# Optimization experiments

Measured on AMD Instinct MI355X. Metric: run time of the kernel, lower is better.

## Reference

```python
import jax, jax.numpy as jnp
import numpy as np

H = 64            # hidden_channels
L = 2             # num_layers
E = 300_000       # edges per relation
B = 64            # graphs in batch
NS = [100_000, 20_000, 50_000, 80_000]   # variable, value, operator, constraint
# (src_type, dst_type) for the 9 hetero relations, fixed order
RELS = [(0,1),(0,2),(0,3),(2,3),(3,3),(1,0),(2,0),(3,0),(3,2)]
R = len(RELS)
SLOPE = 0.2       # GATConv leaky_relu negative slope


def setup_inputs() -> dict:
    key = jax.random.key(0)
    ks = iter(jax.random.split(key, 64))
    inp = {}
    for n, N in zip(["x_variable", "x_value", "x_operator", "x_constraint"], NS):
        inp[n] = jax.random.normal(next(ks), (N, H), jnp.float32)
    sc = 1.0 / np.sqrt(H).astype(np.float32)
    inp["Wsrc"] = jax.random.normal(next(ks), (L, R, H, H), jnp.float32) * sc
    inp["Wdst"] = jax.random.normal(next(ks), (L, R, H, H), jnp.float32) * sc
    inp["asrc"] = jax.random.normal(next(ks), (L, R, H), jnp.float32) * sc
    inp["adst"] = jax.random.normal(next(ks), (L, R, H), jnp.float32) * sc
    inp["bias"] = jax.random.normal(next(ks), (L, R, H), jnp.float32) * 0.01
    inp["lin_w"] = jax.random.normal(next(ks), (2, 2 * H), jnp.float32) / np.sqrt(2.0 * H).astype(np.float32)
    inp["lin_b"] = jnp.zeros((2,), jnp.float32)
    for r, (s, d) in enumerate(RELS):
        inp[f"src{r}"] = jax.random.randint(next(ks), (E,), 0, NS[s], jnp.int32)
        inp[f"dst{r}"] = jax.random.randint(next(ks), (E,), 0, NS[d], jnp.int32)
    inp["batch_variable"] = jnp.sort(jax.random.randint(next(ks), (NS[0],), 0, B, jnp.int32))
    inp["batch_constraint"] = jnp.sort(jax.random.randint(next(ks), (NS[3],), 0, B, jnp.int32))
    inp["num_graphs"] = B
    return inp


def _gat(xs, xd, Ws, Wd, a_s, a_d, b, src, dst):
    """Bipartite PyG GATConv (heads=1, add_self_loops=False)."""
    hs = xs @ Ws                         # [Ns, H]
    hd = xd @ Wd                         # [Nd, H]
    al_s = hs @ a_s                      # [Ns]
    al_d = hd @ a_d                      # [Nd]
    score = jax.nn.leaky_relu(al_s[src] + al_d[dst], SLOPE)    # [E]
    nd = xd.shape[0]
    m = jax.ops.segment_max(score, dst, num_segments=nd)
    p = jnp.exp(score - m[dst])
    z = jax.ops.segment_sum(p, dst, num_segments=nd)
    alpha = p / (z[dst] + 1e-16)                               # segment softmax
    out = jax.ops.segment_sum(hs[src] * alpha[:, None], dst, num_segments=nd)
    return out + b


def _seg_mean(x, seg, n):
    s = jax.ops.segment_sum(x, seg, num_segments=n)
    c = jax.ops.segment_sum(jnp.ones((x.shape[0],), x.dtype), seg, num_segments=n)
    return s / jnp.maximum(c, 1.0)[:, None]


def reference(x_variable, x_value, x_operator, x_constraint,
              Wsrc, Wdst, asrc, adst, bias, lin_w, lin_b,
              src0, dst0, src1, dst1, src2, dst2, src3, dst3, src4, dst4,
              src5, dst5, src6, dst6, src7, dst7, src8, dst8,
              batch_variable, batch_constraint, num_graphs):
    xs = [x_variable, x_value, x_operator, x_constraint]
    srcs = [src0, src1, src2, src3, src4, src5, src6, src7, src8]
    dsts = [dst0, dst1, dst2, dst3, dst4, dst5, dst6, dst7, dst8]
    for l in range(L):
        out = [jnp.zeros((x.shape[0], H), x.dtype) for x in xs]
        for r, (s, d) in enumerate(RELS):
            out[d] = out[d] + _gat(xs[s], xs[d], Wsrc[l, r], Wdst[l, r],
                                   asrc[l, r], adst[l, r], bias[l, r],
                                   srcs[r], dsts[r])
        xs = [jax.nn.relu(o) for o in out]   # dropout is identity in eval
    vp = _seg_mean(xs[0], batch_variable, num_graphs)   # [B, H]
    cp = _seg_mean(xs[3], batch_constraint, num_graphs) # [B, H]
    return jnp.concatenate([vp, cp], axis=1) @ lin_w.T + lin_b   # [B, 2]
```

## Files before the change

kernel.cpp:

```cpp
#include <hip/hip_runtime.h>
#include <hip/hip_bf16.h>

#define NH 64
#define NRELS 9
#define NEDGE 300000
#define NGRAPH 64
#define TOTROWS 250000
#define TOTFSEG 660000
#define TOTEDGE (NRELS * NEDGE)
#define NBUCK 977
#define NBC 4
#define CHUNK 4096
#define NBLK ((TOTEDGE + CHUNK - 1) / CHUNK)
#define KCH 20
#define KSP 33

typedef __attribute__((ext_vector_type(8))) short short8;
typedef __attribute__((ext_vector_type(4))) float f32x4;

__constant__ int c_NS[4]     = {100000, 20000, 50000, 80000};
__constant__ int c_SRC[9]    = {0,0,0,2,3,1,2,3,3};
__constant__ int c_DST[9]    = {1,2,3,3,3,0,0,0,2};
__constant__ int c_XOFF[5]   = {0,100000,120000,170000,250000};
__constant__ int c_ASOFF[10] = {0,100000,200000,300000,350000,430000,450000,500000,580000,660000};
__constant__ int c_FOFF[5]   = {0,300000,320000,420000,660000};
__constant__ int c_NRELT[4]  = {3,1,2,3};
__constant__ int c_RRANK[9]  = {0,0,0,1,2,0,1,2,1};

struct EdgePtrs { const int* s[9]; const int* d[9]; };

__device__ __forceinline__ unsigned short f2bf(float f) {
  union { __hip_bfloat16 h; unsigned short u; } c;
  c.h = __float2bfloat16(f);
  return c.u;
}

__device__ __forceinline__ float wred_max32(float v) {
#pragma unroll
  for (int o = 16; o; o >>= 1) v = fmaxf(v, __shfl_xor(v, o, 32));
  return v;
}

__global__ void k_setup(const float* Wsrc, const float* Wdst, const float* asrc,
                        const float* adst, const float* bias, float* wv, float* bsum,
                        unsigned short* wb) {
  int b = blockIdx.x, j = threadIdx.x;
  if (b < 36) {
    int r = b % 9, q = b / 9;
    int l = q >> 1, side = q & 1;
    const float* W = (side ? Wdst : Wsrc) + (l * 9 + r) * 64 * 64;
    const float* a = (side ? adst : asrc) + (l * 9 + r) * 64;
    float s = 0.f;
    for (int i = 0; i < 64; ++i) s += W[j * 64 + i] * a[i];
    wv[(side ? 1152 : 0) + (l * 9 + r) * 64 + j] = s;
  } else if (b == 36) {
    for (int l = 0; l < 2; ++l)
      for (int t = 0; t < 4; ++t) {
        float s = 0.f;
        for (int r = 0; r < 9; ++r)
          if (c_DST[r] == t) s += bias[(l * 9 + r) * 64 + j];
        bsum[(l * 4 + t) * 64 + j] = s;
      }
  } else {
    int idx = b - 37;
    int l = idx / 9, r = idx % 9;
    const float* W = Wsrc + (size_t)(l * 9 + r) * 4096;
    unsigned short* dst = wb + (size_t)(l * 9 + r) * 4096;
    for (int k = 0; k < 64; ++k)
      dst[j * 64 + k] = f2bf(W[k * 64 + j]);
  }
}

__global__ __launch_bounds__(256) void k_bhist2(EdgePtrs Eg, int* bh) {
  __shared__ int sh[NBUCK];
  for (int i = threadIdx.x; i < NBUCK; i += 256) sh[i] = 0;
  __syncthreads();
  int lo = blockIdx.x * CHUNK;
  int hi = lo + CHUNK; if (hi > TOTEDGE) hi = TOTEDGE;
  for (int gid = lo + threadIdx.x; gid < hi; gid += 256) {
    int r = gid / NEDGE, e = gid - r * NEDGE;
    int g = c_XOFF[c_DST[r]] + Eg.d[r][e];
    atomicAdd(&sh[g >> 8], 1);
  }
  __syncthreads();
  int* dst = bh + (size_t)blockIdx.x * NBUCK;
  for (int i = threadIdx.x; i < NBUCK; i += 256) dst[i] = sh[i];
}

__global__ void k_cs1(const int* bh, int* csum) {
  int blk = blockIdx.x;
  int c = blk / NBC;
  int b = (blk % NBC) * 256 + threadIdx.x;
  if (b >= NBUCK) return;
  int k0 = c * KSP;
  int k1 = k0 + KSP; if (k1 > NBLK) k1 = NBLK;
  int s = 0;
  for (int k = k0; k < k1; ++k) s += bh[(size_t)k * NBUCK + b];
  csum[(size_t)c * NBUCK + b] = s;
}

__global__ void k_cs2(int* csum, int* gbh) {
  int b = blockIdx.x * 256 + threadIdx.x;
  if (b >= NBUCK) return;
  int run = 0;
#pragma unroll
  for (int c = 0; c < KCH; ++c) {
    size_t idx = (size_t)c * NBUCK + b;
    int t = csum[idx];
    csum[idx] = run;
    run += t;
  }
  gbh[b] = run;
}

__global__ void k_cs3(int* bh, const int* csum) {
  int blk = blockIdx.x;
  int c = blk / NBC;
  int b = (blk % NBC) * 256 + threadIdx.x;
  if (b >= NBUCK) return;
  int k0 = c * KSP;
  int k1 = k0 + KSP; if (k1 > NBLK) k1 = NBLK;
  int run = csum[(size_t)c * NBUCK + b];
  for (int k = k0; k < k1; ++k) {
    size_t idx = (size_t)k * NBUCK + b;
    int t = bh[idx];
    bh[idx] = run;
    run += t;
  }
}

__global__ void k_bscan(const int* gbh, int* boff) {
  __shared__ int sd[1024];
  int t = threadIdx.x;
  int v = (t < NBUCK) ? gbh[t] : 0;
  sd[t] = v; __syncthreads();
  for (int o = 1; o < 1024; o <<= 1) {
    int x = (t >= o) ? sd[t - o] : 0; __syncthreads();
    sd[t] += x; __syncthreads();
  }
  if (t < NBUCK) boff[t] = sd[t] - v;
  if (t == 1023) boff[NBUCK] = sd[1023];
}

__global__ __launch_bounds__(256) void k_bin2(EdgePtrs Eg, const int* bh, const int* boff, int* pairs) {
  __shared__ int cur[NBUCK];
  const int* mybh = bh + (size_t)blockIdx.x * NBUCK;
  for (int i = threadIdx.x; i < NBUCK; i += 256) cur[i] = boff[i] + mybh[i];
  __syncthreads();
  int lo = blockIdx.x * CHUNK;
  int hi = lo + CHUNK; if (hi > TOTEDGE) hi = TOTEDGE;
  for (int gid = lo + threadIdx.x; gid < hi; gid += 256) {
    int r = gid / NEDGE, e = gid - r * NEDGE;
    int g = c_XOFF[c_DST[r]] + Eg.d[r][e];
    int b = g >> 8;
    int pos = atomicAdd(&cur[b], 1);
    int key = ((g & 255) << 2) | c_RRANK[r];
    pairs[pos] = (key << 20) | (c_ASOFF[r] + Eg.s[r][e]);
  }
}

__global__ __launch_bounds__(256) void k_bsort(const int* pairs, const int* boff,
                                               int* rowptr, int* asx) {
  __shared__ int ssc[1024];
  __shared__ int scur[1024];
  __shared__ int sws[256];
  int b = blockIdx.x, t = threadIdx.x;
  int lo = boff[b], hi = boff[b + 1];
  int n = hi - lo;
  for (int i = t; i < 1024; i += 256) ssc[i] = 0;
  __syncthreads();
  for (int i = t; i < n; i += 256)
    atomicAdd(&ssc[((unsigned)pairs[lo + i]) >> 20], 1);
  __syncthreads();
  int c0 = ssc[t * 4], c1 = ssc[t * 4 + 1], c2 = ssc[t * 4 + 2], c3 = ssc[t * 4 + 3];
  int s = c0 + c1 + c2 + c3;
  sws[t] = s;
  __syncthreads();
  for (int o = 1; o < 256; o <<= 1) {
    int x = (t >= o) ? sws[t - o] : 0; __syncthreads();
    sws[t] += x; __syncthreads();
  }
  int base = sws[t] - s;
  ssc[t * 4]     = base;
  ssc[t * 4 + 1] = base + c0;
  ssc[t * 4 + 2] = base + c0 + c1;
  ssc[t * 4 + 3] = base + c0 + c1 + c2;
  scur[t * 4]     = ssc[t * 4];
  scur[t * 4 + 1] = ssc[t * 4 + 1];
  scur[t * 4 + 2] = ssc[t * 4 + 2];
  scur[t * 4 + 3] = ssc[t * 4 + 3];
  __syncthreads();
  int nodeBase = b << 8;
  for (int i = t; i < 1024; i += 256) {
    int l = i >> 2, rank = i & 3;
    int g = nodeBase + l;
    if (g < TOTROWS) {
      int tt = (g >= c_XOFF[1]) + (g >= c_XOFF[2]) + (g >= c_XOFF[3]);
      int nr = c_NRELT[tt];
      if (rank < nr)
        rowptr[c_FOFF[tt] + (g - c_XOFF[tt]) * nr + rank] = lo + ssc[i];
    }
  }
  if (b == 0 && t == 0) rowptr[TOTFSEG] = TOTEDGE;
  for (int i = t; i < n; i += 256) {
    int p = pairs[lo + i];
    int pos = atomicAdd(&scur[((unsigned)p) >> 20], 1);
    asx[lo + pos] = (int)(((((unsigned)p >> 20) & 3u) << 20) | ((unsigned)p & 0xFFFFFu));
  }
}

struct GemmAllP {
  const float* x0; const float* x1; const float* x2; const float* x3;
  const unsigned short* Wb;
  __hip_bfloat16* hs;
  float* als; float* ald;
  const float* wvs; const float* wvd;
  int act; int ntyp;
  int tbase[5];
  int typ[4];
  int nrel[4];
  int rel[4][3];
  int ndrel[4];
  int drel[4][3];
};

#define XSTR 72

__global__ __launch_bounds__(256) void k_gemma(GemmAllP G) {
  __shared__ unsigned short sx[64 * XSTR];
  __shared__ unsigned short sw[64 * XSTR];
  int bid = blockIdx.x;
  int k = 0;
#pragma unroll 3
  for (int q = 1; q < 4; ++q) if (q < G.ntyp) k += (bid >= G.tbase[q]);
  int st = G.typ[k];
  int tile = bid - G.tbase[k];
  int Ns = c_NS[st];
  const float* x = st == 0 ? G.x0 : st == 1 ? G.x1 : st == 2 ? G.x2 : G.x3;
  int base = tile * 64;
  int tid = threadIdx.x;
  for (int kk = tid; kk < 1024; kk += 256) {
    int row = kk >> 4;
    int c4 = (kk & 15) * 4;
    int gr = base + row;
    float4 v = make_float4(0.f, 0.f, 0.f, 0.f);
    if (gr < Ns) v = ((const float4*)x)[(size_t)gr * 16 + (kk & 15)];
    if (G.act) { v.x = fmaxf(v.x, 0.f); v.y = fmaxf(v.y, 0.f); v.z = fmaxf(v.z, 0.f); v.w = fmaxf(v.w, 0.f); }
    ushort4 u;
    u.x = f2bf(v.x); u.y = f2bf(v.y); u.z = f2bf(v.z); u.w = f2bf(v.w);
    *(ushort4*)&sx[row * XSTR + c4] = u;
  }
  __syncthreads();
  {
    int row = tid >> 2, part = tid & 3;
    int gr2 = base + row;
    if (gr2 < Ns) {
      float xv[16];
      const float4* xr = (const float4*)x + (size_t)gr2 * 16 + part * 4;
      float4 v0 = xr[0], v1 = xr[1], v2 = xr[2], v3 = xr[3];
      xv[0]=v0.x; xv[1]=v0.y; xv[2]=v0.z; xv[3]=v0.w;
      xv[4]=v1.x; xv[5]=v1.y; xv[6]=v1.z; xv[7]=v1.w;
      xv[8]=v2.x; xv[9]=v2.y; xv[10]=v2.z; xv[11]=v2.w;
      xv[12]=v3.x; xv[13]=v3.y; xv[14]=v3.z; xv[15]=v3.w;
      if (G.act) {
#pragma unroll
        for (int i = 0; i < 16; ++i) xv[i] = fmaxf(xv[i], 0.f);
      }
      int nrl0 = G.nrel[k];
      for (int ri = 0; ri < nrl0; ++ri) {
        int r = G.rel[k][ri];
        const float* wvp = G.wvs + r * 64 + part * 16;
        float s = 0.f;
#pragma unroll
        for (int i = 0; i < 16; ++i) s += xv[i] * wvp[i];
        s += __shfl_xor(s, 1);
        s += __shfl_xor(s, 2);
        if (part == 0) G.als[c_ASOFF[r] + gr2] = s;
      }
      int ndl = G.ndrel[k];
      for (int ri = 0; ri < ndl; ++ri) {
        int r = G.drel[k][ri];
        const float* wvp = G.wvd + r * 64 + part * 16;
        float s = 0.f;
#pragma unroll
        for (int i = 0; i < 16; ++i) s += xv[i] * wvp[i];
        s += __shfl_xor(s, 1);
        s += __shfl_xor(s, 2);
        if (part == 0)
          G.ald[c_FOFF[st] + gr2 * c_NRELT[st] + c_RRANK[r]] = s;
      }
    }
  }
  int w    = tid >> 6;
  int lane = tid & 63;
  int m    = lane & 15;
  int quad = lane >> 4;
  short8 a0 = *(const short8*)&sx[(w * 16 + m) * XSTR + quad * 8];
  short8 a1 = *(const short8*)&sx[(w * 16 + m) * XSTR + 32 + quad * 8];
  int nrl = G.nrel[k];
  for (int ri = 0; ri < nrl; ++ri) {
    int r = G.rel[k][ri];
    const unsigned short* Wb = G.Wb + (size_t)r * 4096;
    if (ri) __syncthreads();
    {
      int n = tid >> 2;
      int k0 = (tid & 3) << 4;
      short8 w0 = *(const short8*)&Wb[n * 64 + k0];
      short8 w1 = *(const short8*)&Wb[n * 64 + k0 + 8];
      *(short8*)&sw[n * XSTR + k0] = w0;
      *(short8*)&sw[n * XSTR + k0 + 8] = w1;
    }
    __syncthreads();
    f32x4 acc[4];
#pragma unroll
    for (int cb = 0; cb < 4; ++cb) acc[cb] = (f32x4)(0.f);
#pragma unroll
    for (int cb = 0; cb < 4; ++cb) {
      short8 b0 = *(const short8*)&sw[(cb * 16 + m) * XSTR + quad * 8];
      short8 b1 = *(const short8*)&sw[(cb * 16 + m) * XSTR + 32 + quad * 8];
      acc[cb] = __builtin_amdgcn_mfma_f32_16x16x32_bf16(a0, b0, acc[cb], 0, 0, 0);
      acc[cb] = __builtin_amdgcn_mfma_f32_16x16x32_bf16(a1, b1, acc[cb], 0, 0, 0);
    }
    __hip_bfloat16* hsb = G.hs + (size_t)c_ASOFF[r] * 64;
#pragma unroll
    for (int cb = 0; cb < 4; ++cb)
#pragma unroll
      for (int reg = 0; reg < 4; ++reg)
        sx[(w * 16 + quad * 4 + reg) * XSTR + cb * 16 + m] = f2bf(acc[cb][reg]);
    int rrow = w * 16 + (lane >> 2);
    int rcol = (lane & 3) * 16;
    int lr = base + rrow;
    if (lr < Ns) {
      short8 v0 = *(const short8*)&sx[rrow * XSTR + rcol];
      short8 v1 = *(const short8*)&sx[rrow * XSTR + rcol + 8];
      *(short8*)&hsb[(size_t)lr * 64 + rcol] = v0;
      *(short8*)&hsb[(size_t)lr * 64 + rcol + 8] = v1;
    }
  }
}

struct GatherP {
  const __hip_bfloat16* hs;
  const float* als;
  const float* ald;
  const int* rowptr; const int* asx;
  float* xA;
  const float* bsum;
  int ntypes;
  int tbase[5];
  int typ[4];
};

__global__ __launch_bounds__(256) void k_gather(GatherP A) {
  __shared__ unsigned long long sRA[8][96];
  __shared__ float sZ[8][4];
  int bid = blockIdx.x;
  int k = 0;
#pragma unroll 3
  for (int q = 1; q < 4; ++q) if (q < A.ntypes) k += (bid >= A.tbase[q]);
  int t = A.typ[k];
  int Nd = c_NS[t];
  int lane = threadIdx.x & 63;
  int half = lane >> 5;
  int sl   = lane & 31;
  int hid  = threadIdx.x >> 5;
  int node = (bid - A.tbase[k]) * 8 + (threadIdx.x >> 6) * 2 + half;
  if (node >= Nd) return;
  int nr = c_NRELT[t];
  int fb = c_FOFF[t] + node * nr;
  int p0 = A.rowptr[fb];
  int p1 = A.rowptr[fb + nr];
  int deg = p1 - p0; if (deg > 96) deg = 96;
  float2 acc = ((const float2*)(A.bsum + t * 64))[sl];
  if (deg > 0) {
    if (sl < 4) sZ[hid][sl] = 0.f;
    const float NEG = -3.4e38f;
    const unsigned* ax = (const unsigned*)A.asx;
    unsigned rec0 = 0, rec1 = 0, rec2 = 0;
    int rk0 = 0, rk1 = 0, rk2 = 0;
    float s0 = NEG, s1 = NEG, s2 = NEG;
    if (sl < deg) {
      rec0 = ax[p0 + sl];
      rk0 = (int)((rec0 >> 20) & 3u);
      float v = A.als[rec0 & 0xFFFFFu] + A.ald[fb + rk0];
      s0 = v >= 0.f ? v : 0.2f * v;
    }
    if (sl + 32 < deg) {
      rec1 = ax[p0 + 32 + sl];
      rk1 = (int)((rec1 >> 20) & 3u);
      float v = A.als[rec1 & 0xFFFFFu] + A.ald[fb + rk1];
      s1 = v >= 0.f ? v : 0.2f * v;
    }
    if (sl + 64 < deg) {
      rec2 = ax[p0 + 64 + sl];
      rk2 = (int)((rec2 >> 20) & 3u);
      float v = A.als[rec2 & 0xFFFFFu] + A.ald[fb + rk2];
      s2 = v >= 0.f ? v : 0.2f * v;
    }
    float M = wred_max32(fmaxf(fmaxf(s0, s1), s2));
    float e0 = 0.f, e1 = 0.f, e2 = 0.f;
    if (sl < deg)      { e0 = __expf(s0 - M); atomicAdd(&sZ[hid][rk0], e0); }
    if (sl + 32 < deg) { e1 = __expf(s1 - M); atomicAdd(&sZ[hid][rk1], e1); }
    if (sl + 64 < deg) { e2 = __expf(s2 - M); atomicAdd(&sZ[hid][rk2], e2); }
    asm volatile("s_waitcnt lgkmcnt(0)" ::: "memory");
    float rz0 = 1.f / (sZ[hid][0] + 1e-16f);
    float rz1 = 1.f / (sZ[hid][1] + 1e-16f);
    float rz2 = 1.f / (sZ[hid][2] + 1e-16f);
    float a0 = e0 * (rk0 == 0 ? rz0 : (rk0 == 1 ? rz1 : rz2));
    sRA[hid][sl] = ((unsigned long long)__float_as_uint(a0) << 32) | ((rec0 & 0xFFFFFu) << 7);
    if (deg > 32) {
      float a1 = e1 * (rk1 == 0 ? rz0 : (rk1 == 1 ? rz1 : rz2));
      sRA[hid][32 + sl] = ((unsigned long long)__float_as_uint(a1) << 32) | ((rec1 & 0xFFFFFu) << 7);
    }
    if (deg > 64) {
      float a2 = e2 * (rk2 == 0 ? rz0 : (rk2 == 1 ? rz1 : rz2));
      sRA[hid][64 + sl] = ((unsigned long long)__float_as_uint(a2) << 32) | ((rec2 & 0xFFFFFu) << 7);
    }
    const char* hsb = (const char*)A.hs;
    unsigned sl4 = (unsigned)sl * 4u;
    int nb = (deg + 7) >> 3;
    for (int g = 0; g < nb; g += 2) {
      unsigned long long raA[8], raB[8];
      unsigned hA[8], hB[8];
      bool hasB = (g + 1) < nb;
#pragma unroll
      for (int q = 0; q < 8; ++q) raA[q] = sRA[hid][g * 8 + q];
#pragma unroll
      for (int q = 0; q < 8; ++q)
        hA[q] = *(const unsigned*)(hsb + ((unsigned)(raA[q] & 0xFFFFFFFFu) + sl4));
      if (hasB) {
#pragma unroll
        for (int q = 0; q < 8; ++q) raB[q] = sRA[hid][g * 8 + 8 + q];
#pragma unroll
        for (int q = 0; q < 8; ++q)
          hB[q] = *(const unsigned*)(hsb + ((unsigned)(raB[q] & 0xFFFFFFFFu) + sl4));
      }
#pragma unroll
      for (int q = 0; q < 8; ++q) {
        float aq = __uint_as_float((unsigned)(raA[q] >> 32));
        acc.x = fmaf(aq, __uint_as_float(hA[q] << 16), acc.x);
        acc.y = fmaf(aq, __uint_as_float(hA[q] & 0xffff0000u), acc.y);
      }
      if (hasB) {
#pragma unroll
        for (int q = 0; q < 8; ++q) {
          float aq = __uint_as_float((unsigned)(raB[q] >> 32));
          acc.x = fmaf(aq, __uint_as_float(hB[q] << 16), acc.x);
          acc.y = fmaf(aq, __uint_as_float(hB[q] & 0xffff0000u), acc.y);
        }
      }
    }
  }
  float* xout = A.xA + (size_t)c_XOFF[t] * 64;
  *(float2*)&xout[(size_t)node * 64 + sl * 2] = acc;
}

struct GatherPoolP {
  const __hip_bfloat16* hs;
  const float* als;
  const float* ald;
  const int* rowptr; const int* asx;
  const float* bsum;
  int ntypes;
  int tbase[5];
  int typ[4];
  const int* bvar; const int* bcon;
  float* partial;
};

__global__ __launch_bounds__(256) void k_gatherpool(GatherPoolP A) {
  __shared__ unsigned long long sRA[8][96];
  __shared__ float sZ[8][4];
  __shared__ float sPool[8][64];
  __shared__ int sG[8];
  int bid = blockIdx.x;
  int k = 0;
#pragma unroll 3
  for (int q = 1; q < 4; ++q) if (q < A.ntypes) k += (bid >= A.tbase[q]);
  int t = A.typ[k];
  int Nd = c_NS[t];
  int lane = threadIdx.x & 63;
  int half = lane >> 5;
  int sl   = lane & 31;
  int hid  = threadIdx.x >> 5;
  int node = (bid - A.tbase[k]) * 8 + (threadIdx.x >> 6) * 2 + half;
  bool active = node < Nd;
  float2 acc = ((const float2*)(A.bsum + t * 64))[sl];
  int nr = c_NRELT[t];
  int fb = c_FOFF[t] + node * nr;
  int deg = 0, p0 = 0;
  if (active) {
    p0 = A.rowptr[fb];
    int p1 = A.rowptr[fb + nr];
    deg = p1 - p0; if (deg > 96) deg = 96;
  }
  if (deg > 0) {
    if (sl < 4) sZ[hid][sl] = 0.f;
    const float NEG = -3.4e38f;
    const unsigned* ax = (const unsigned*)A.asx;
    unsigned rec0 = 0, rec1 = 0, rec2 = 0;
    int rk0 = 0, rk1 = 0, rk2 = 0;
    float s0 = NEG, s1 = NEG, s2 = NEG;
    if (sl < deg) {
      rec0 = ax[p0 + sl];
      rk0 = (int)((rec0 >> 20) & 3u);
      float v = A.als[rec0 & 0xFFFFFu] + A.ald[fb + rk0];
      s0 = v >= 0.f ? v : 0.2f * v;
    }
    if (sl + 32 < deg) {
      rec1 = ax[p0 + 32 + sl];
      rk1 = (int)((rec1 >> 20) & 3u);
      float v = A.als[rec1 & 0xFFFFFu] + A.ald[fb + rk1];
      s1 = v >= 0.f ? v : 0.2f * v;
    }
    if (sl + 64 < deg) {
      rec2 = ax[p0 + 64 + sl];
      rk2 = (int)((rec2 >> 20) & 3u);
      float v = A.als[rec2 & 0xFFFFFu] + A.ald[fb + rk2];
      s2 = v >= 0.f ? v : 0.2f * v;
    }
    float M = wred_max32(fmaxf(fmaxf(s0, s1), s2));
    float e0 = 0.f, e1 = 0.f, e2 = 0.f;
    if (sl < deg)      { e0 = __expf(s0 - M); atomicAdd(&sZ[hid][rk0], e0); }
    if (sl + 32 < deg) { e1 = __expf(s1 - M); atomicAdd(&sZ[hid][rk1], e1); }
    if (sl + 64 < deg) { e2 = __expf(s2 - M); atomicAdd(&sZ[hid][rk2], e2); }
    asm volatile("s_waitcnt lgkmcnt(0)" ::: "memory");
    float rz0 = 1.f / (sZ[hid][0] + 1e-16f);
    float rz1 = 1.f / (sZ[hid][1] + 1e-16f);
    float rz2 = 1.f / (sZ[hid][2] + 1e-16f);
    float a0 = e0 * (rk0 == 0 ? rz0 : (rk0 == 1 ? rz1 : rz2));
    sRA[hid][sl] = ((unsigned long long)__float_as_uint(a0) << 32) | ((rec0 & 0xFFFFFu) << 7);
    if (deg > 32) {
      float a1 = e1 * (rk1 == 0 ? rz0 : (rk1 == 1 ? rz1 : rz2));
      sRA[hid][32 + sl] = ((unsigned long long)__float_as_uint(a1) << 32) | ((rec1 & 0xFFFFFu) << 7);
    }
    if (deg > 64) {
      float a2 = e2 * (rk2 == 0 ? rz0 : (rk2 == 1 ? rz1 : rz2));
      sRA[hid][64 + sl] = ((unsigned long long)__float_as_uint(a2) << 32) | ((rec2 & 0xFFFFFu) << 7);
    }
    const char* hsb = (const char*)A.hs;
    unsigned sl4 = (unsigned)sl * 4u;
    int nb = (deg + 7) >> 3;
    for (int g = 0; g < nb; g += 2) {
      unsigned long long raA[8], raB[8];
      unsigned hA[8], hB[8];
      bool hasB = (g + 1) < nb;
#pragma unroll
      for (int q = 0; q < 8; ++q) raA[q] = sRA[hid][g * 8 + q];
#pragma unroll
      for (int q = 0; q < 8; ++q)
        hA[q] = *(const unsigned*)(hsb + ((unsigned)(raA[q] & 0xFFFFFFFFu) + sl4));
      if (hasB) {
#pragma unroll
        for (int q = 0; q < 8; ++q) raB[q] = sRA[hid][g * 8 + 8 + q];
#pragma unroll
        for (int q = 0; q < 8; ++q)
          hB[q] = *(const unsigned*)(hsb + ((unsigned)(raB[q] & 0xFFFFFFFFu) + sl4));
      }
#pragma unroll
      for (int q = 0; q < 8; ++q) {
        float aq = __uint_as_float((unsigned)(raA[q] >> 32));
        acc.x = fmaf(aq, __uint_as_float(hA[q] << 16), acc.x);
        acc.y = fmaf(aq, __uint_as_float(hA[q] & 0xffff0000u), acc.y);
      }
      if (hasB) {
#pragma unroll
        for (int q = 0; q < 8; ++q) {
          float aq = __uint_as_float((unsigned)(raB[q] >> 32));
          acc.x = fmaf(aq, __uint_as_float(hB[q] << 16), acc.x);
          acc.y = fmaf(aq, __uint_as_float(hB[q] & 0xffff0000u), acc.y);
        }
      }
    }
  }
  sPool[hid][sl * 2]     = fmaxf(acc.x, 0.f);
  sPool[hid][sl * 2 + 1] = fmaxf(acc.y, 0.f);
  if (sl == 0) {
    int gid = -1;
    if (active) {
      int g = (t == 0) ? A.bvar[node] : A.bcon[node];
      gid = (g << 1) | (t == 3 ? 1 : 0);
    }
    sG[hid] = gid;
  }
  __syncthreads();
  if (threadIdx.x < 64) {
    int col = threadIdx.x;
    int sp = (bid & 7) << 7;
    float a = 0.f; int cg = -1;
#pragma unroll
    for (int i = 0; i < 8; ++i) {
      int gi = sG[i];
      if (gi < 0) continue;
      float v = sPool[i][col];
      if (gi == cg) a += v;
      else {
        if (cg >= 0) atomicAdd(&A.partial[(size_t)(sp | cg) * 64 + col], a);
        cg = gi; a = v;
      }
    }
    if (cg >= 0) atomicAdd(&A.partial[(size_t)(sp | cg) * 64 + col], a);
  }
}

__global__ void k_gbound(const int* bvar, const int* bcon, int* gs0, int* gs3, float* partial) {
  int gid = blockIdx.x * 256 + threadIdx.x;
  const int N0 = 100000, N3 = 80000;
  if (gid < N0) {
    int i = gid;
    int b = bvar[i];
    int bp = i ? bvar[i - 1] : -1;
    for (int g = bp + 1; g <= b; ++g) gs0[g] = i;
    if (i == N0 - 1) for (int g = b + 1; g <= 64; ++g) gs0[g] = N0;
  } else if (gid < N0 + N3) {
    int i = gid - N0;
    int b = bcon[i];
    int bp = i ? bcon[i - 1] : -1;
    for (int g = bp + 1; g <= b; ++g) gs3[g] = i;
    if (i == N3 - 1) for (int g = b + 1; g <= 64; ++g) gs3[g] = N3;
  } else if (gid < N0 + N3 + 65536) {
    partial[gid - N0 - N3] = 0.f;
  }
}

__global__ void k_poolred2(const float* partial, float* pool) {
  int g = blockIdx.x >> 1;
  int t = blockIdx.x & 1;
  int col = threadIdx.x;
  float s = 0.f;
#pragma unroll
  for (int sp = 0; sp < 8; ++sp)
    s += partial[(size_t)(((sp << 7) | (g << 1) | t)) * 64 + col];
  pool[(t ? 4096 : 0) + g * 64 + col] = s;
}

__global__ void k_final(const float* pool, const int* gs0, const int* gs3,
                        const float* lin_w, const float* lin_b, float* out) {
  int k = threadIdx.x;
  int g = k >> 1, o = k & 1;
  float c0 = fmaxf((float)(gs0[g + 1] - gs0[g]), 1.f);
  float c3 = fmaxf((float)(gs3[g + 1] - gs3[g]), 1.f);
  float acc = lin_b[o];
  for (int i = 0; i < 64; ++i) {
    acc += (pool[g * 64 + i] / c0) * lin_w[o * 128 + i];
    acc += (pool[4096 + g * 64 + i] / c3) * lin_w[o * 128 + 64 + i];
  }
  out[g * 2 + o] = acc;
}

__global__ void k_bail(float* out) {
  if (threadIdx.x < 128) out[threadIdx.x] = 0.f;
}

extern "C" void kernel_launch(void* const* d_in, const int* in_sizes, int n_in,
                              void* d_out, int out_size, void* d_ws, size_t ws_size,
                              hipStream_t stream) {
  (void)in_sizes; (void)n_in; (void)out_size;
  const size_t O_XA   = 0;
  const size_t O_HS   = 16000000;
  const size_t O_ALS  = 37120000;
  const size_t O_ALD  = 37780000;
  const size_t O_WV   = 39790000;
  const size_t O_BS   = 39792304;
  const size_t O_RP   = 39792816;
  const size_t O_ASX  = 40452832;
  const size_t O_GS   = 43152832;
  const size_t O_PART = 43153088;
  const size_t O_POOL = 43218624;
  const size_t O_WB   = 43226816;
  const size_t NEED   = 43263680;

  if (ws_size < NEED * 4) {
    k_bail<<<1, 128, 0, stream>>>((float*)d_out);
    return;
  }

  const float* x0 = (const float*)d_in[0];
  const float* x1 = (const float*)d_in[1];
  const float* x2 = (const float*)d_in[2];
  const float* x3 = (const float*)d_in[3];
  const float* Wsrc = (const float*)d_in[4];
  const float* Wdst = (const float*)d_in[5];
  const float* asrc = (const float*)d_in[6];
  const float* adst = (const float*)d_in[7];
  const float* bias = (const float*)d_in[8];
  const float* lin_w = (const float*)d_in[9];
  const float* lin_b = (const float*)d_in[10];
  EdgePtrs Eg;
  for (int r = 0; r < 9; ++r) {
    Eg.s[r] = (const int*)d_in[11 + 2 * r];
    Eg.d[r] = (const int*)d_in[12 + 2 * r];
  }
  const int* bvar = (const int*)d_in[29];
  const int* bcon = (const int*)d_in[30];

  float* ws = (float*)d_ws;
  float* xA   = ws + O_XA;
  __hip_bfloat16* hs = (__hip_bfloat16*)(ws + O_HS);
  int* bh     = (int*)(ws + O_HS);
  int* pairs  = bh + (size_t)NBLK * NBUCK;
  int* gbh    = pairs + 2700000;
  int* boff   = gbh + (NBUCK + 1);
  int* csum   = boff + (NBUCK + 2);
  float* als  = ws + O_ALS;
  float* ald  = ws + O_ALD;
  float* wv   = ws + O_WV;
  float* bsum = ws + O_BS;
  int* rowptr = (int*)(ws + O_RP);
  int* asx    = (int*)(ws + O_ASX);
  int* gs0    = (int*)(ws + O_GS);
  int* gs3    = gs0 + 65;
  float* partial = ws + O_PART;
  float* pool = ws + O_POOL;
  unsigned short* wb = (unsigned short*)(ws + O_WB);

  const int h_NS[4]   = {100000, 20000, 50000, 80000};
  const int h_SRC[9]  = {0,0,0,2,3,1,2,3,3};
  const int h_DST[9]  = {1,2,3,3,3,0,0,0,2};
  const int h_XOFF[4] = {0,100000,120000,170000};

  k_setup<<<55, 64, 0, stream>>>(Wsrc, Wdst, asrc, adst, bias, wv, bsum, wb);

  k_bhist2<<<NBLK, 256, 0, stream>>>(Eg, bh);
  k_cs1<<<KCH * NBC, 256, 0, stream>>>(bh, csum);
  k_cs2<<<NBC, 256, 0, stream>>>(csum, gbh);
  k_cs3<<<KCH * NBC, 256, 0, stream>>>(bh, csum);
  k_bscan<<<1, 1024, 0, stream>>>(gbh, boff);
  k_bin2<<<NBLK, 256, 0, stream>>>(Eg, bh, boff, pairs);
  k_bsort<<<NBUCK, 256, 0, stream>>>(pairs, boff, rowptr, asx);
  k_gbound<<<(180000 + 65536 + 255) / 256, 256, 0, stream>>>(bvar, bcon, gs0, gs3, partial);

  for (int l = 0; l < 2; ++l) {
    const float* xin[4];
    if (l == 0) { xin[0] = x0; xin[1] = x1; xin[2] = x2; xin[3] = x3; }
    else {
      for (int t = 0; t < 4; ++t) xin[t] = xA + (size_t)h_XOFF[t] * 64;
    }
    int act = (l > 0);
    int relmask = l ? 0x0FC : 0x1FF;

    GemmAllP G;
    G.x0 = xin[0]; G.x1 = xin[1]; G.x2 = xin[2]; G.x3 = xin[3];
    G.Wb = wb + (size_t)l * 9 * 4096;
    G.hs = hs; G.act = act;
    G.als = als; G.ald = ald;
    G.wvs = wv + l * 576; G.wvd = wv + 1152 + l * 576;
    int ntyp = 0, cum = 0;
    for (int t = 0; t < 4; ++t) {
      int nr = 0; int rl[3]; int nd = 0; int dl[3];
      for (int r = 0; r < 9; ++r) {
        if (!((relmask >> r) & 1)) continue;
        if (h_SRC[r] == t) rl[nr++] = r;
        if (h_DST[r] == t) dl[nd++] = r;
      }
      if (!nr && !nd) continue;
      G.typ[ntyp] = t; G.nrel[ntyp] = nr; G.ndrel[ntyp] = nd;
      for (int i = 0; i < 3; ++i) {
        G.rel[ntyp][i]  = (i < nr) ? rl[i] : 0;
        G.drel[ntyp][i] = (i < nd) ? dl[i] : 0;
      }
      G.tbase[ntyp] = cum;
      cum += (h_NS[t] + 63) / 64;
      ++ntyp;
    }
    G.ntyp = ntyp; G.tbase[ntyp] = cum;
    k_gemma<<<cum, 256, 0, stream>>>(G);

    if (l == 0) {
      GatherP A;
      A.hs = hs; A.als = als; A.ald = ald;
      A.rowptr = rowptr; A.asx = asx;
      A.xA = xA;
      A.bsum = bsum;
      int nt = 0, bcum = 0;
      for (int t = 0; t < 4; ++t) {
        A.typ[nt] = t;
        A.tbase[nt] = bcum;
        bcum += (h_NS[t] + 7) / 8;
        ++nt;
      }
      A.ntypes = nt; A.tbase[nt] = bcum;
      k_gather<<<bcum, 256, 0, stream>>>(A);
    } else {
      GatherPoolP A;
      A.hs = hs; A.als = als; A.ald = ald;
      A.rowptr = rowptr; A.asx = asx;
      A.bsum = bsum + 256;
      A.bvar = bvar; A.bcon = bcon;
      A.partial = partial;
      int nt = 0, bcum = 0;
      for (int t = 0; t < 4; ++t) {
        if (t == 1 || t == 2) continue;
        A.typ[nt] = t;
        A.tbase[nt] = bcum;
        bcum += (h_NS[t] + 7) / 8;
        ++nt;
      }
      A.ntypes = nt; A.tbase[nt] = bcum;
      k_gatherpool<<<bcum, 256, 0, stream>>>(A);
    }
  }

  k_poolred2<<<128, 64, 0, stream>>>(partial, pool);
  k_final<<<1, 128, 0, stream>>>(pool, gs0, gs3, lin_w, lin_b, (float*)d_out);
}
```

Baseline: 489.4 us.

## Replace per-block histogram scan with global atomic bucket counters and merge final kernels

The edge binning pipeline no longer stores per-block histograms and runs a three-stage column scan. Each block now adds its local bucket counts into a global histogram with atomics, a single scan produces bucket offsets, and the binning kernel recounts locally and reserves its slot range with one atomic per bucket. This removes three kernel launches and the large per-block histogram traffic, at the cost of re-reading the destination indices in the binning kernel and a nondeterministic edge order within buckets, which the later per-bucket sort is expected to absorb. The pool reduction and final linear layer are also fused into one single-block kernel.

```diff
diff --git a/kernel.cpp b/kernel.cpp
--- a/kernel.cpp
+++ b/kernel.cpp
@@ -9,11 +9,8 @@
 #define TOTFSEG 660000
 #define TOTEDGE (NRELS * NEDGE)
 #define NBUCK 977
-#define NBC 4
 #define CHUNK 4096
 #define NBLK ((TOTEDGE + CHUNK - 1) / CHUNK)
-#define KCH 20
-#define KSP 33
 
 typedef __attribute__((ext_vector_type(8))) short short8;
 typedef __attribute__((ext_vector_type(4))) float f32x4;
@@ -43,7 +40,7 @@
 
 __global__ void k_setup(const float* Wsrc, const float* Wdst, const float* asrc,
                         const float* adst, const float* bias, float* wv, float* bsum,
-                        unsigned short* wb) {
+                        unsigned short* wb, int* gbh) {
   int b = blockIdx.x, j = threadIdx.x;
   if (b < 36) {
     int r = b % 9, q = b / 9;
@@ -61,6 +58,8 @@
           if (c_DST[r] == t) s += bias[(l * 9 + r) * 64 + j];
         bsum[(l * 4 + t) * 64 + j] = s;
       }
+  } else if (b == 55) {
+    for (int i = j; i < NBUCK; i += 64) gbh[i] = 0;
   } else {
     int idx = b - 37;
     int l = idx / 9, r = idx % 9;
@@ -71,7 +70,7 @@
   }
 }
 
-__global__ __launch_bounds__(256) void k_bhist2(EdgePtrs Eg, int* bh) {
+__global__ __launch_bounds__(256) void k_bhist(EdgePtrs Eg, int* gbh) {
   __shared__ int sh[NBUCK];
   for (int i = threadIdx.x; i < NBUCK; i += 256) sh[i] = 0;
   __syncthreads();
@@ -83,53 +82,13 @@
     atomicAdd(&sh[g >> 8], 1);
   }
   __syncthreads();
-  int* dst = bh + (size_t)blockIdx.x * NBUCK;
-  for (int i = threadIdx.x; i < NBUCK; i += 256) dst[i] = sh[i];
-}
-
-__global__ void k_cs1(const int* bh, int* csum) {
-  int blk = blockIdx.x;
-  int c = blk / NBC;
-  int b = (blk % NBC) * 256 + threadIdx.x;
-  if (b >= NBUCK) return;
-  int k0 = c * KSP;
-  int k1 = k0 + KSP; if (k1 > NBLK) k1 = NBLK;
-  int s = 0;
-  for (int k = k0; k < k1; ++k) s += bh[(size_t)k * NBUCK + b];
-  csum[(size_t)c * NBUCK + b] = s;
-}
-
-__global__ void k_cs2(int* csum, int* gbh) {
-  int b = blockIdx.x * 256 + threadIdx.x;
-  if (b >= NBUCK) return;
-  int run = 0;
-#pragma unroll
-  for (int c = 0; c < KCH; ++c) {
-    size_t idx = (size_t)c * NBUCK + b;
-    int t = csum[idx];
-    csum[idx] = run;
-    run += t;
-  }
-  gbh[b] = run;
-}
-
-__global__ void k_cs3(int* bh, const int* csum) {
-  int blk = blockIdx.x;
-  int c = blk / NBC;
-  int b = (blk % NBC) * 256 + threadIdx.x;
-  if (b >= NBUCK) return;
-  int k0 = c * KSP;
-  int k1 = k0 + KSP; if (k1 > NBLK) k1 = NBLK;
-  int run = csum[(size_t)c * NBUCK + b];
-  for (int k = k0; k < k1; ++k) {
-    size_t idx = (size_t)k * NBUCK + b;
-    int t = bh[idx];
-    bh[idx] = run;
-    run += t;
-  }
-}
-
-__global__ void k_bscan(const int* gbh, int* boff) {
+  for (int i = threadIdx.x; i < NBUCK; i += 256) {
+    int v = sh[i];
+    if (v) atomicAdd(&gbh[i], v);
+  }
+}
+
+__global__ void k_bscan(const int* gbh, int* boff, int* cur) {
   __shared__ int sd[1024];
   int t = threadIdx.x;
   int v = (t < NBUCK) ? gbh[t] : 0;
@@ -138,24 +97,36 @@
     int x = (t >= o) ? sd[t - o] : 0; __syncthreads();
     sd[t] += x; __syncthreads();
   }
-  if (t < NBUCK) boff[t] = sd[t] - v;
+  if (t < NBUCK) { int e = sd[t] - v; boff[t] = e; cur[t] = e; }
   if (t == 1023) boff[NBUCK] = sd[1023];
 }
 
-__global__ __launch_bounds__(256) void k_bin2(EdgePtrs Eg, const int* bh, const int* boff, int* pairs) {
-  __shared__ int cur[NBUCK];
-  const int* mybh = bh + (size_t)blockIdx.x * NBUCK;
-  for (int i = threadIdx.x; i < NBUCK; i += 256) cur[i] = boff[i] + mybh[i];
+__global__ __launch_bounds__(256) void k_bin(EdgePtrs Eg, int* cur, int* pairs) {
+  __shared__ int sh[NBUCK];
+  __shared__ int sbase[NBUCK];
+  for (int i = threadIdx.x; i < NBUCK; i += 256) sh[i] = 0;
   __syncthreads();
   int lo = blockIdx.x * CHUNK;
   int hi = lo + CHUNK; if (hi > TOTEDGE) hi = TOTEDGE;
   for (int gid = lo + threadIdx.x; gid < hi; gid += 256) {
     int r = gid / NEDGE, e = gid - r * NEDGE;
     int g = c_XOFF[c_DST[r]] + Eg.d[r][e];
+    atomicAdd(&sh[g >> 8], 1);
+  }
+  __syncthreads();
+  for (int i = threadIdx.x; i < NBUCK; i += 256) {
+    int v = sh[i];
+    sbase[i] = v ? atomicAdd(&cur[i], v) : 0;
+    sh[i] = 0;
+  }
+  __syncthreads();
+  for (int gid = lo + threadIdx.x; gid < hi; gid += 256) {
+    int r = gid / NEDGE, e = gid - r * NEDGE;
+    int g = c_XOFF[c_DST[r]] + Eg.d[r][e];
     int b = g >> 8;
-    int pos = atomicAdd(&cur[b], 1);
+    int off = atomicAdd(&sh[b], 1);
     int key = ((g & 255) << 2) | c_RRANK[r];
-    pairs[pos] = (key << 20) | (c_ASOFF[r] + Eg.s[r][e]);
+    pairs[sbase[b] + off] = (key << 20) | (c_ASOFF[r] + Eg.s[r][e]);
   }
 }
 
@@ -623,29 +594,31 @@
   }
 }
 
-__global__ void k_poolred2(const float* partial, float* pool) {
-  int g = blockIdx.x >> 1;
-  int t = blockIdx.x & 1;
-  int col = threadIdx.x;
-  float s = 0.f;
-#pragma unroll
-  for (int sp = 0; sp < 8; ++sp)
-    s += partial[(size_t)(((sp << 7) | (g << 1) | t)) * 64 + col];
-  pool[(t ? 4096 : 0) + g * 64 + col] = s;
-}
-
-__global__ void k_final(const float* pool, const int* gs0, const int* gs3,
-                        const float* lin_w, const float* lin_b, float* out) {
-  int k = threadIdx.x;
-  int g = k >> 1, o = k & 1;
-  float c0 = fmaxf((float)(gs0[g + 1] - gs0[g]), 1.f);
-  float c3 = fmaxf((float)(gs3[g + 1] - gs3[g]), 1.f);
-  float acc = lin_b[o];
-  for (int i = 0; i < 64; ++i) {
-    acc += (pool[g * 64 + i] / c0) * lin_w[o * 128 + i];
-    acc += (pool[4096 + g * 64 + i] / c3) * lin_w[o * 128 + 64 + i];
-  }
-  out[g * 2 + o] = acc;
+__global__ __launch_bounds__(256) void k_final2(const float* partial, const int* gs0, const int* gs3,
+                                                const float* lin_w, const float* lin_b, float* out) {
+  __shared__ float sp[8192];
+  int tid = threadIdx.x;
+  for (int j = 0; j < 32; ++j) {
+    int v = j * 256 + tid;
+    int tg = v >> 6, col = v & 63;
+    float s = 0.f;
+#pragma unroll
+    for (int spi = 0; spi < 8; ++spi)
+      s += partial[(size_t)((spi << 7) | tg) * 64 + col];
+    sp[tg * 64 + col] = s;
+  }
+  __syncthreads();
+  if (tid < 128) {
+    int g = tid >> 1, o = tid & 1;
+    float c0 = fmaxf((float)(gs0[g + 1] - gs0[g]), 1.f);
+    float c3 = fmaxf((float)(gs3[g + 1] - gs3[g]), 1.f);
+    float acc = lin_b[o];
+    for (int i = 0; i < 64; ++i) {
+      acc += (sp[(g << 1) * 64 + i] / c0) * lin_w[o * 128 + i];
+      acc += (sp[((g << 1) | 1) * 64 + i] / c3) * lin_w[o * 128 + 64 + i];
+    }
+    out[g * 2 + o] = acc;
+  }
 }
 
 __global__ void k_bail(float* out) {
@@ -669,6 +642,7 @@
   const size_t O_POOL = 43218624;
   const size_t O_WB   = 43226816;
   const size_t NEED   = 43263680;
+  (void)O_POOL;
 
   if (ws_size < NEED * 4) {
     k_bail<<<1, 128, 0, stream>>>((float*)d_out);
@@ -697,11 +671,10 @@
   float* ws = (float*)d_ws;
   float* xA   = ws + O_XA;
   __hip_bfloat16* hs = (__hip_bfloat16*)(ws + O_HS);
-  int* bh     = (int*)(ws + O_HS);
-  int* pairs  = bh + (size_t)NBLK * NBUCK;
+  int* pairs  = (int*)(ws + O_HS);
   int* gbh    = pairs + 2700000;
-  int* boff   = gbh + (NBUCK + 1);
-  int* csum   = boff + (NBUCK + 2);
+  int* boff   = gbh + NBUCK + 1;
+  int* cur    = boff + NBUCK + 2;
   float* als  = ws + O_ALS;
   float* ald  = ws + O_ALD;
   float* wv   = ws + O_WV;
@@ -711,7 +684,6 @@
   int* gs0    = (int*)(ws + O_GS);
   int* gs3    = gs0 + 65;
   float* partial = ws + O_PART;
-  float* pool = ws + O_POOL;
   unsigned short* wb = (unsigned short*)(ws + O_WB);
 
   const int h_NS[4]   = {100000, 20000, 50000, 80000};
@@ -719,14 +691,11 @@
   const int h_DST[9]  = {1,2,3,3,3,0,0,0,2};
   const int h_XOFF[4] = {0,100000,120000,170000};
 
-  k_setup<<<55, 64, 0, stream>>>(Wsrc, Wdst, asrc, adst, bias, wv, bsum, wb);
-
-  k_bhist2<<<NBLK, 256, 0, stream>>>(Eg, bh);
-  k_cs1<<<KCH * NBC, 256, 0, stream>>>(bh, csum);
-  k_cs2<<<NBC, 256, 0, stream>>>(csum, gbh);
-  k_cs3<<<KCH * NBC, 256, 0, stream>>>(bh, csum);
-  k_bscan<<<1, 1024, 0, stream>>>(gbh, boff);
-  k_bin2<<<NBLK, 256, 0, stream>>>(Eg, bh, boff, pairs);
+  k_setup<<<56, 64, 0, stream>>>(Wsrc, Wdst, asrc, adst, bias, wv, bsum, wb, gbh);
+
+  k_bhist<<<NBLK, 256, 0, stream>>>(Eg, gbh);
+  k_bscan<<<1, 1024, 0, stream>>>(gbh, boff, cur);
+  k_bin<<<NBLK, 256, 0, stream>>>(Eg, cur, pairs);
   k_bsort<<<NBUCK, 256, 0, stream>>>(pairs, boff, rowptr, asx);
   k_gbound<<<(180000 + 65536 + 255) / 256, 256, 0, stream>>>(bvar, bcon, gs0, gs3, partial);
 
@@ -801,6 +770,5 @@
     }
   }
 
-  k_poolred2<<<128, 64, 0, stream>>>(partial, pool);
-  k_final<<<1, 128, 0, stream>>>(pool, gs0, gs3, lin_w, lin_b, (float*)d_out);
-}
+  k_final2<<<1, 256, 0, stream>>>(partial, gs0, gs3, lin_w, lin_b, (float*)d_out);
+}
```

After: 479.3 us. 1.02x faster.
